# Kernel tuning notes

Hardware: AMD Instinct MI355X
Metric: run time of the kernel (lower is better)

## Reference

```python
import jax, jax.numpy as jnp
import numpy as np

B, T, U, D, V = 8, 200, 100, 512, 1024


def setup_inputs() -> dict:
    key = jax.random.key(0)
    k1, k2, k3, k4 = jax.random.split(key, 4)
    enc_out = jax.random.normal(k1, (B, T, D), dtype=jnp.float32)
    prefix = jax.random.randint(k2, (B, U), 0, V, dtype=jnp.int64)
    embedding = jax.random.normal(k3, (V, D), dtype=jnp.float32)
    joiner_w = jax.random.normal(k4, (V, D), dtype=jnp.float32) * (1.0 / np.sqrt(D))
    joiner_b = jnp.zeros((V,), dtype=jnp.float32)
    return {"enc_out": enc_out, "prefix": prefix, "embedding": embedding,
            "joiner_w": joiner_w, "joiner_b": joiner_b}


def reference(enc_out, prefix, embedding, joiner_w, joiner_b):
    # pred_emb: (B, U, D) via embedding lookup
    pred_emb = embedding[prefix]
    # broadcast add -> (B, T, U, D), then tanh
    joint = jnp.tanh(enc_out[:, :, None, :] + pred_emb[:, None, :, :])
    # linear projection to vocab: (B, T, U, V)
    logits = jnp.einsum('btud,vd->btuv', joint, joiner_w) + joiner_b
    return logits
```

## Files before the change

kernel.cpp:

```cpp
#include <hip/hip_runtime.h>

#define T_DIM 200
#define U_DIM 100
#define D_DIM 512
#define V_DIM 1024
#define TU_DIM (T_DIM * U_DIM)
#define M_TOTAL (8 * TU_DIM)
#define M_TILE 64

typedef __attribute__((ext_vector_type(8))) short bf16x8;
typedef __attribute__((ext_vector_type(4))) float f32x4;

__device__ __forceinline__ unsigned short f2bf(float f) {
    unsigned int u = __float_as_uint(f);
    u += 0x7FFFu + ((u >> 16) & 1u);
    return (unsigned short)(u >> 16);
}

__device__ __forceinline__ float fast_tanh(float x) {
    float e = __expf(2.0f * x);
    return 1.0f - 2.0f / (e + 1.0f);
}

__device__ __forceinline__ void row_ptrs(int g, const float* enc, const int* prefix,
                                         const float* emb, const float** encp, const float** embp) {
    const int b = g / TU_DIM;
    const int m = g - b * TU_DIM;
    const int t = m / U_DIM;
    const int u = m - t * U_DIM;
    *encp = enc + (size_t)(b * T_DIM + t) * D_DIM;
    *embp = emb + (size_t)prefix[b * U_DIM + u] * D_DIM;
}

__global__ void conv_w_kernel(const float* __restrict__ w, ushort4* __restrict__ wbf) {
    int i = blockIdx.x * blockDim.x + threadIdx.x;
    float4 v = reinterpret_cast<const float4*>(w)[i];
    ushort4 o;
    o.x = f2bf(v.x); o.y = f2bf(v.y); o.z = f2bf(v.z); o.w = f2bf(v.w);
    wbf[i] = o;
}

__global__ __launch_bounds__(512)
void mat_a_kernel(const float* __restrict__ enc, const int* __restrict__ prefix,
                  const float* __restrict__ emb, unsigned short* __restrict__ Abf) {
    const int tid = threadIdx.x;
    const int r = tid >> 3;
    const int q = tid & 7;
    const int rl = blockIdx.x * 64 + r;
    const float *encp, *embp;
    row_ptrs(rl, enc, prefix, emb, &encp, &embp);
    unsigned short* ap = Abf + (size_t)rl * D_DIM;
#pragma unroll
    for (int jj = 0; jj < 8; ++jj) {
        const int d = q * 8 + jj * 64;
        float4 e0 = *reinterpret_cast<const float4*>(encp + d);
        float4 e1 = *reinterpret_cast<const float4*>(encp + d + 4);
        float4 p0 = *reinterpret_cast<const float4*>(embp + d);
        float4 p1 = *reinterpret_cast<const float4*>(embp + d + 4);
        bf16x8 pk;
        pk[0] = (short)f2bf(fast_tanh(e0.x + p0.x));
        pk[1] = (short)f2bf(fast_tanh(e0.y + p0.y));
        pk[2] = (short)f2bf(fast_tanh(e0.z + p0.z));
        pk[3] = (short)f2bf(fast_tanh(e0.w + p0.w));
        pk[4] = (short)f2bf(fast_tanh(e1.x + p1.x));
        pk[5] = (short)f2bf(fast_tanh(e1.y + p1.y));
        pk[6] = (short)f2bf(fast_tanh(e1.z + p1.z));
        pk[7] = (short)f2bf(fast_tanh(e1.w + p1.w));
        *reinterpret_cast<bf16x8*>(&ap[d]) = pk;
    }
}

#define GLOAD_LDS16(gp, lp) \
    __builtin_amdgcn_global_load_lds( \
        (const __attribute__((address_space(1))) unsigned int*)(gp), \
        (__attribute__((address_space(3))) unsigned int*)(lp), 16, 0, 0)

__global__ __launch_bounds__(256, 2)
void gemm128_kernel(const unsigned short* __restrict__ Abf, const unsigned short* __restrict__ wbf,
                    const float* __restrict__ bias, float* __restrict__ out) {
    __shared__ unsigned short ldsA[2][128 * 64];
    __shared__ unsigned short ldsB[2][128 * 64];

    const int tid  = threadIdx.x;
    const int lane = tid & 63;
    const int wid  = tid >> 6;
    const int wm   = (wid >> 1) * 64;
    const int wn   = (wid & 1) * 64;
    const int lr   = lane & 15;
    const int lg   = lane >> 4;

    const int orig = blockIdx.x;
    const int wgid = (orig & 7) * 1250 + (orig >> 3);
    const int mt = wgid >> 3, nt = wgid & 7;
    const int row0 = mt * 128, col0 = nt * 128;

    const int rsub = tid >> 3;
    const int csw  = ((tid & 7) ^ (rsub & 7)) * 8;
    const unsigned short* aSt = Abf + (size_t)(row0 + rsub) * D_DIM + csw;
    const unsigned short* wSt = wbf + (size_t)(col0 + rsub) * D_DIM + csw;

    auto stage = [&](int buf, int kt) {
        const int k0 = kt * 64;
#pragma unroll
        for (int i = 0; i < 4; ++i)
            GLOAD_LDS16(aSt + (size_t)(i * 32) * D_DIM + k0,
                        &ldsA[buf][(i * 32 + wid * 8) * 64]);
#pragma unroll
        for (int i = 0; i < 4; ++i)
            GLOAD_LDS16(wSt + (size_t)(i * 32) * D_DIM + k0,
                        &ldsB[buf][(i * 32 + wid * 8) * 64]);
    };

    const unsigned short* ldsA0 = &ldsA[0][(wm + lr) * 64 + ((lg ^ (lr & 7)) * 8)];
    const unsigned short* ldsB0 = &ldsB[0][(wn + lr) * 64 + ((lg ^ (lr & 7)) * 8)];
    const int kk1off = ((((4 | lg) ^ (lr & 7)) - (lg ^ (lr & 7))) * 8);

    f32x4 acc[4][4];
#pragma unroll
    for (int mi = 0; mi < 4; ++mi)
#pragma unroll
        for (int ni = 0; ni < 4; ++ni)
            acc[mi][ni] = (f32x4){0.f, 0.f, 0.f, 0.f};

    auto compute = [&](int buf) {
        const unsigned short* pA = ldsA0 + buf * (128 * 64);
        const unsigned short* pB = ldsB0 + buf * (128 * 64);
#pragma unroll
        for (int kk = 0; kk < 2; ++kk) {
            const int ko = kk ? kk1off : 0;
            bf16x8 bfr[4];
#pragma unroll
            for (int ni = 0; ni < 4; ++ni)
                bfr[ni] = *reinterpret_cast<const bf16x8*>(pB + ni * (16 * 64) + ko);
            __builtin_amdgcn_s_setprio(1);
#pragma unroll
            for (int mi = 0; mi < 4; ++mi) {
                bf16x8 af = *reinterpret_cast<const bf16x8*>(pA + mi * (16 * 64) + ko);
#pragma unroll
                for (int ni = 0; ni < 4; ++ni)
                    acc[mi][ni] = __builtin_amdgcn_mfma_f32_16x16x32_bf16(af, bfr[ni], acc[mi][ni], 0, 0, 0);
            }
            __builtin_amdgcn_s_setprio(0);
        }
    };

    stage(0, 0);
    stage(1, 1);

#pragma unroll 1
    for (int it = 0; it < 4; ++it) {
        asm volatile("s_waitcnt vmcnt(8)" ::: "memory");
        __builtin_amdgcn_s_barrier();
        compute(0);
        asm volatile("s_waitcnt lgkmcnt(0)" ::: "memory");
        __builtin_amdgcn_s_barrier();
        if (it < 3) stage(0, 2 * it + 2);
        if (it < 3) asm volatile("s_waitcnt vmcnt(8)" ::: "memory");
        else        asm volatile("s_waitcnt vmcnt(0)" ::: "memory");
        __builtin_amdgcn_s_barrier();
        compute(1);
        if (it < 3) {
            asm volatile("s_waitcnt lgkmcnt(0)" ::: "memory");
            __builtin_amdgcn_s_barrier();
            stage(1, 2 * it + 3);
        }
    }

    float bv[4];
#pragma unroll
    for (int ni = 0; ni < 4; ++ni)
        bv[ni] = bias[col0 + wn + ni * 16 + lr];
#pragma unroll
    for (int mi = 0; mi < 4; ++mi) {
#pragma unroll
        for (int j = 0; j < 4; ++j) {
            const long long row = (long long)row0 + wm + mi * 16 + lg * 4 + j;
            float* op = out + row * V_DIM + col0 + wn;
#pragma unroll
            for (int ni = 0; ni < 4; ++ni)
                __builtin_nontemporal_store(acc[mi][ni][j] + bv[ni], &op[ni * 16 + lr]);
        }
    }
}

__global__ __launch_bounds__(512, 2)
void joiner_kernel(const float* __restrict__ enc, const int* __restrict__ prefix,
                   const float* __restrict__ emb, const unsigned short* __restrict__ wbf,
                   const float* __restrict__ bias, float* __restrict__ out) {
    __shared__ unsigned short A_s[M_TILE * 512];
    const int tid = threadIdx.x;
    const long long g0 = (long long)blockIdx.x * M_TILE;
    {
        const int r = tid >> 3, q = tid & 7;
        const float *encp, *embp;
        row_ptrs((int)g0 + r, enc, prefix, emb, &encp, &embp);
        const int r7 = r & 7;
#pragma unroll
        for (int jj = 0; jj < 8; ++jj) {
            const int d = q * 8 + jj * 64;
            float4 e0 = *reinterpret_cast<const float4*>(encp + d);
            float4 e1 = *reinterpret_cast<const float4*>(encp + d + 4);
            float4 p0 = *reinterpret_cast<const float4*>(embp + d);
            float4 p1 = *reinterpret_cast<const float4*>(embp + d + 4);
            bf16x8 pk;
            pk[0] = (short)f2bf(fast_tanh(e0.x + p0.x));
            pk[1] = (short)f2bf(fast_tanh(e0.y + p0.y));
            pk[2] = (short)f2bf(fast_tanh(e0.z + p0.z));
            pk[3] = (short)f2bf(fast_tanh(e0.w + p0.w));
            pk[4] = (short)f2bf(fast_tanh(e1.x + p1.x));
            pk[5] = (short)f2bf(fast_tanh(e1.y + p1.y));
            pk[6] = (short)f2bf(fast_tanh(e1.z + p1.z));
            pk[7] = (short)f2bf(fast_tanh(e1.w + p1.w));
            const int chunk = (q + 8 * jj) ^ r7;
            *reinterpret_cast<bf16x8*>(&A_s[r * 512 + chunk * 8]) = pk;
        }
    }
    __syncthreads();
    const int lane = tid & 63, wid = tid >> 6;
    const int wn = wid * 128, lr = lane & 15, lg = lane >> 4;
    const unsigned short* wb = wbf + (size_t)(wn + lr) * D_DIM + lg * 8;
    f32x4 acc[4][8];
#pragma unroll
    for (int mi = 0; mi < 4; ++mi)
#pragma unroll
        for (int ni = 0; ni < 8; ++ni) acc[mi][ni] = (f32x4){0.f, 0.f, 0.f, 0.f};
    bf16x8 bb[2][8];
#pragma unroll
    for (int ni = 0; ni < 8; ++ni)
        bb[0][ni] = *reinterpret_cast<const bf16x8*>(wb + ni * 16 * D_DIM);
#pragma unroll
    for (int s = 0; s < 16; ++s) {
        const int cur = s & 1, nxt = cur ^ 1;
        if (s < 15) {
#pragma unroll
            for (int ni = 0; ni < 8; ++ni)
                bb[nxt][ni] = *reinterpret_cast<const bf16x8*>(wb + ni * 16 * D_DIM + (s + 1) * 32);
        }
        bf16x8 af[4];
#pragma unroll
        for (int mi = 0; mi < 4; ++mi) {
            const int row = mi * 16 + lr;
            const int chunk = (s * 4 + lg) ^ (row & 7);
            af[mi] = *reinterpret_cast<const bf16x8*>(&A_s[row * 512 + chunk * 8]);
        }
#pragma unroll
        for (int mi = 0; mi < 4; ++mi)
#pragma unroll
            for (int ni = 0; ni < 8; ++ni)
                acc[mi][ni] = __builtin_amdgcn_mfma_f32_16x16x32_bf16(af[mi], bb[cur][ni], acc[mi][ni], 0, 0, 0);
    }
    float bv[8];
#pragma unroll
    for (int ni = 0; ni < 8; ++ni) bv[ni] = bias[wn + ni * 16 + lr];
#pragma unroll
    for (int mi = 0; mi < 4; ++mi) {
#pragma unroll
        for (int j = 0; j < 4; ++j) {
            const long long row = g0 + mi * 16 + lg * 4 + j;
            float* op = out + row * V_DIM + wn;
#pragma unroll
            for (int ni = 0; ni < 8; ++ni)
                op[ni * 16 + lr] = acc[mi][ni][j] + bv[ni];
        }
    }
}

extern "C" void kernel_launch(void* const* d_in, const int* in_sizes, int n_in,
                              void* d_out, int out_size, void* d_ws, size_t ws_size,
                              hipStream_t stream) {
    const float* enc    = (const float*)d_in[0];
    const int*   prefix = (const int*)d_in[1];
    const float* emb    = (const float*)d_in[2];
    const float* jw     = (const float*)d_in[3];
    const float* jb     = (const float*)d_in[4];
    float* out = (float*)d_out;

    unsigned short* wbf = (unsigned short*)d_ws;
    const size_t WB = (size_t)V_DIM * D_DIM * sizeof(unsigned short);
    const size_t AB = (size_t)M_TOTAL * D_DIM * sizeof(unsigned short);

    conv_w_kernel<<<512, 256, 0, stream>>>(jw, (ushort4*)wbf);

    if (ws_size >= WB + AB) {
        unsigned short* Abf = wbf + (size_t)V_DIM * D_DIM;
        mat_a_kernel<<<M_TOTAL / 64, 512, 0, stream>>>(enc, prefix, emb, Abf);
        gemm128_kernel<<<10000, 256, 0, stream>>>(Abf, wbf, jb, out);
    } else {
        joiner_kernel<<<M_TOTAL / M_TILE, 512, 0, stream>>>(enc, prefix, emb, wbf, jb, out);
    }
}
```

Baseline: 276.5 us.

## Prefetch whole LDS k-tile into registers before issuing next stage and MFMAs

The GEMM main loop now reads both k-halves of the A and B fragments for the current buffer into registers, then waits on LDS reads and immediately issues the global-to-LDS load for the next tile into the same buffer before running the MFMAs. This lets the next tile's global loads overlap the whole MFMA block and removes one barrier per tile. The cost is higher register pressure from holding 16 fragments. The tanh/bf16 pre-pass also switches its packed store to a nontemporal store.

```diff
diff --git a/kernel.cpp b/kernel.cpp
--- a/kernel.cpp
+++ b/kernel.cpp
@@ -66,7 +66,7 @@
         pk[5] = (short)f2bf(fast_tanh(e1.y + p1.y));
         pk[6] = (short)f2bf(fast_tanh(e1.z + p1.z));
         pk[7] = (short)f2bf(fast_tanh(e1.w + p1.w));
-        *reinterpret_cast<bf16x8*>(&ap[d]) = pk;
+        __builtin_nontemporal_store(pk, reinterpret_cast<bf16x8*>(&ap[d]));
     }
 }
 
@@ -122,47 +122,45 @@
         for (int ni = 0; ni < 4; ++ni)
             acc[mi][ni] = (f32x4){0.f, 0.f, 0.f, 0.f};
 
-    auto compute = [&](int buf) {
+    stage(0, 0);
+    stage(1, 1);
+    asm volatile("s_waitcnt vmcnt(8)" ::: "memory");
+    __builtin_amdgcn_s_barrier();
+
+#pragma unroll 1
+    for (int it = 0; it < 8; ++it) {
+        const int buf = it & 1;
         const unsigned short* pA = ldsA0 + buf * (128 * 64);
         const unsigned short* pB = ldsB0 + buf * (128 * 64);
+        bf16x8 fa[2][4], fb[2][4];
 #pragma unroll
         for (int kk = 0; kk < 2; ++kk) {
             const int ko = kk ? kk1off : 0;
-            bf16x8 bfr[4];
+#pragma unroll
+            for (int mi = 0; mi < 4; ++mi)
+                fa[kk][mi] = *reinterpret_cast<const bf16x8*>(pA + mi * (16 * 64) + ko);
 #pragma unroll
             for (int ni = 0; ni < 4; ++ni)
-                bfr[ni] = *reinterpret_cast<const bf16x8*>(pB + ni * (16 * 64) + ko);
-            __builtin_amdgcn_s_setprio(1);
-#pragma unroll
-            for (int mi = 0; mi < 4; ++mi) {
-                bf16x8 af = *reinterpret_cast<const bf16x8*>(pA + mi * (16 * 64) + ko);
-#pragma unroll
-                for (int ni = 0; ni < 4; ++ni)
-                    acc[mi][ni] = __builtin_amdgcn_mfma_f32_16x16x32_bf16(af, bfr[ni], acc[mi][ni], 0, 0, 0);
-            }
-            __builtin_amdgcn_s_setprio(0);
-        }
-    };
-
-    stage(0, 0);
-    stage(1, 1);
-
-#pragma unroll 1
-    for (int it = 0; it < 4; ++it) {
-        asm volatile("s_waitcnt vmcnt(8)" ::: "memory");
-        __builtin_amdgcn_s_barrier();
-        compute(0);
+                fb[kk][ni] = *reinterpret_cast<const bf16x8*>(pB + ni * (16 * 64) + ko);
+        }
         asm volatile("s_waitcnt lgkmcnt(0)" ::: "memory");
         __builtin_amdgcn_s_barrier();
-        if (it < 3) stage(0, 2 * it + 2);
-        if (it < 3) asm volatile("s_waitcnt vmcnt(8)" ::: "memory");
-        else        asm volatile("s_waitcnt vmcnt(0)" ::: "memory");
-        __builtin_amdgcn_s_barrier();
-        compute(1);
-        if (it < 3) {
-            asm volatile("s_waitcnt lgkmcnt(0)" ::: "memory");
+        if (it < 6) stage(buf, it + 2);
+        __builtin_amdgcn_s_setprio(1);
+#pragma unroll
+        for (int kk = 0; kk < 2; ++kk)
+#pragma unroll
+            for (int mi = 0; mi < 4; ++mi)
+#pragma unroll
+                for (int ni = 0; ni < 4; ++ni)
+                    acc[mi][ni] = __builtin_amdgcn_mfma_f32_16x16x32_bf16(fa[kk][mi], fb[kk][ni], acc[mi][ni], 0, 0, 0);
+        __builtin_amdgcn_s_setprio(0);
+        if (it < 6) {
+            asm volatile("s_waitcnt vmcnt(8)" ::: "memory");
             __builtin_amdgcn_s_barrier();
-            stage(1, 2 * it + 3);
+        } else if (it == 6) {
+            asm volatile("s_waitcnt vmcnt(0)" ::: "memory");
+            __builtin_amdgcn_s_barrier();
         }
     }
 
```

New measurement: 383.7 us. 1.39x slower.

## Fuse weight conversion, activation prep and GEMM into one cooperative persistent kernel

Applied to the files above, without the earlier changes.

Replaces the three launches (weight bf16 conversion, tanh activation matrix build, tiled GEMM) with a single cooperative kernel of 512 persistent blocks. The blocks do the conversion and the A-matrix build, synchronise with a grid-wide barrier, then loop over the GEMM tiles. The output stores become nontemporal. This removes launch gaps and tail effects between stages, in exchange for a grid sync and fewer resident blocks, which may lower latency hiding in the GEMM phase. The old launch path remains as a fallback if the cooperative launch fails.

```diff
diff --git a/kernel.cpp b/kernel.cpp
--- a/kernel.cpp
+++ b/kernel.cpp
@@ -1,4 +1,7 @@
 #include <hip/hip_runtime.h>
+#include <hip/hip_cooperative_groups.h>
+
+namespace cg = cooperative_groups;
 
 #define T_DIM 200
 #define U_DIM 100
@@ -7,6 +10,8 @@
 #define TU_DIM (T_DIM * U_DIM)
 #define M_TOTAL (8 * TU_DIM)
 #define M_TILE 64
+#define NTILES 10000
+#define PBLK 512
 
 typedef __attribute__((ext_vector_type(8))) short bf16x8;
 typedef __attribute__((ext_vector_type(4))) float f32x4;
@@ -30,6 +35,162 @@
     const int u = m - t * U_DIM;
     *encp = enc + (size_t)(b * T_DIM + t) * D_DIM;
     *embp = emb + (size_t)prefix[b * U_DIM + u] * D_DIM;
+}
+
+__device__ __forceinline__ void mat_a_row8(const float* encp, const float* embp,
+                                           unsigned short* ap, int d) {
+    float4 e0 = *reinterpret_cast<const float4*>(encp + d);
+    float4 e1 = *reinterpret_cast<const float4*>(encp + d + 4);
+    float4 p0 = *reinterpret_cast<const float4*>(embp + d);
+    float4 p1 = *reinterpret_cast<const float4*>(embp + d + 4);
+    bf16x8 pk;
+    pk[0] = (short)f2bf(fast_tanh(e0.x + p0.x));
+    pk[1] = (short)f2bf(fast_tanh(e0.y + p0.y));
+    pk[2] = (short)f2bf(fast_tanh(e0.z + p0.z));
+    pk[3] = (short)f2bf(fast_tanh(e0.w + p0.w));
+    pk[4] = (short)f2bf(fast_tanh(e1.x + p1.x));
+    pk[5] = (short)f2bf(fast_tanh(e1.y + p1.y));
+    pk[6] = (short)f2bf(fast_tanh(e1.z + p1.z));
+    pk[7] = (short)f2bf(fast_tanh(e1.w + p1.w));
+    *reinterpret_cast<bf16x8*>(&ap[d]) = pk;
+}
+
+#define GLOAD_LDS16(gp, lp) \
+    __builtin_amdgcn_global_load_lds( \
+        (const __attribute__((address_space(1))) unsigned int*)(gp), \
+        (__attribute__((address_space(3))) unsigned int*)(lp), 16, 0, 0)
+
+__global__ __launch_bounds__(256, 2)
+void fused_kernel(const float* __restrict__ enc, const int* __restrict__ prefix,
+                  const float* __restrict__ emb, const float* __restrict__ w,
+                  const float* __restrict__ bias, float* __restrict__ out,
+                  unsigned short* __restrict__ wbf, unsigned short* __restrict__ Abf) {
+    __shared__ unsigned short ldsA[2][128 * 64];
+    __shared__ unsigned short ldsB[2][128 * 64];
+
+    const int tid  = threadIdx.x;
+    const int lane = tid & 63;
+    const int wid  = tid >> 6;
+    const int wm   = (wid >> 1) * 64;
+    const int wn   = (wid & 1) * 64;
+    const int lr   = lane & 15;
+    const int lg   = lane >> 4;
+
+    {
+        const int i = blockIdx.x * 256 + tid;
+        float4 v = reinterpret_cast<const float4*>(w)[i];
+        ushort4 o;
+        o.x = f2bf(v.x); o.y = f2bf(v.y); o.z = f2bf(v.z); o.w = f2bf(v.w);
+        reinterpret_cast<ushort4*>(wbf)[i] = o;
+        const int rsub8 = tid >> 3;
+        const int q = tid & 7;
+        for (int g = blockIdx.x; g < 5000; g += PBLK) {
+            const int rl = g * 32 + rsub8;
+            const float *encp, *embp;
+            row_ptrs(rl, enc, prefix, emb, &encp, &embp);
+            unsigned short* ap = Abf + (size_t)rl * D_DIM;
+#pragma unroll
+            for (int jj = 0; jj < 8; ++jj)
+                mat_a_row8(encp, embp, ap, q * 8 + jj * 64);
+        }
+    }
+    __threadfence();
+    cg::this_grid().sync();
+
+    const int rsub = tid >> 3;
+    const int csw  = ((tid & 7) ^ (rsub & 7)) * 8;
+    const unsigned short* ldsA0 = &ldsA[0][(wm + lr) * 64 + ((lg ^ (lr & 7)) * 8)];
+    const unsigned short* ldsB0 = &ldsB[0][(wn + lr) * 64 + ((lg ^ (lr & 7)) * 8)];
+    const int kk1off = ((((4 | lg) ^ (lr & 7)) - (lg ^ (lr & 7))) * 8);
+
+#pragma unroll 1
+    for (int tile = blockIdx.x; tile < NTILES; tile += PBLK) {
+        const int wgid = (tile & 7) * 1250 + (tile >> 3);
+        const int mt = wgid >> 3, nt = wgid & 7;
+        const int row0 = mt * 128, col0 = nt * 128;
+
+        const unsigned short* aSt = Abf + (size_t)(row0 + rsub) * D_DIM + csw;
+        const unsigned short* wSt = wbf + (size_t)(col0 + rsub) * D_DIM + csw;
+
+        auto stage = [&](int buf, int kt) {
+            const int k0 = kt * 64;
+#pragma unroll
+            for (int i = 0; i < 4; ++i)
+                GLOAD_LDS16(aSt + (size_t)(i * 32) * D_DIM + k0,
+                            &ldsA[buf][(i * 32 + wid * 8) * 64]);
+#pragma unroll
+            for (int i = 0; i < 4; ++i)
+                GLOAD_LDS16(wSt + (size_t)(i * 32) * D_DIM + k0,
+                            &ldsB[buf][(i * 32 + wid * 8) * 64]);
+        };
+
+        f32x4 acc[4][4];
+#pragma unroll
+        for (int mi = 0; mi < 4; ++mi)
+#pragma unroll
+            for (int ni = 0; ni < 4; ++ni)
+                acc[mi][ni] = (f32x4){0.f, 0.f, 0.f, 0.f};
+
+        auto compute = [&](int buf) {
+            const unsigned short* pA = ldsA0 + buf * (128 * 64);
+            const unsigned short* pB = ldsB0 + buf * (128 * 64);
+#pragma unroll
+            for (int kk = 0; kk < 2; ++kk) {
+                const int ko = kk ? kk1off : 0;
+                bf16x8 bfr[4];
+#pragma unroll
+                for (int ni = 0; ni < 4; ++ni)
+                    bfr[ni] = *reinterpret_cast<const bf16x8*>(pB + ni * (16 * 64) + ko);
+                __builtin_amdgcn_s_setprio(1);
+#pragma unroll
+                for (int mi = 0; mi < 4; ++mi) {
+                    bf16x8 af = *reinterpret_cast<const bf16x8*>(pA + mi * (16 * 64) + ko);
+#pragma unroll
+                    for (int ni = 0; ni < 4; ++ni)
+                        acc[mi][ni] = __builtin_amdgcn_mfma_f32_16x16x32_bf16(af, bfr[ni], acc[mi][ni], 0, 0, 0);
+                }
+                __builtin_amdgcn_s_setprio(0);
+            }
+        };
+
+        stage(0, 0);
+        stage(1, 1);
+#pragma unroll 1
+        for (int it = 0; it < 4; ++it) {
+            asm volatile("s_waitcnt vmcnt(8)" ::: "memory");
+            __builtin_amdgcn_s_barrier();
+            compute(0);
+            asm volatile("s_waitcnt lgkmcnt(0)" ::: "memory");
+            __builtin_amdgcn_s_barrier();
+            if (it < 3) stage(0, 2 * it + 2);
+            if (it < 3) asm volatile("s_waitcnt vmcnt(8)" ::: "memory");
+            else        asm volatile("s_waitcnt vmcnt(0)" ::: "memory");
+            __builtin_amdgcn_s_barrier();
+            compute(1);
+            if (it < 3) {
+                asm volatile("s_waitcnt lgkmcnt(0)" ::: "memory");
+                __builtin_amdgcn_s_barrier();
+                stage(1, 2 * it + 3);
+            }
+        }
+
+        float bv[4];
+#pragma unroll
+        for (int ni = 0; ni < 4; ++ni)
+            bv[ni] = bias[col0 + wn + ni * 16 + lr];
+#pragma unroll
+        for (int mi = 0; mi < 4; ++mi) {
+#pragma unroll
+            for (int j = 0; j < 4; ++j) {
+                const long long row = (long long)row0 + wm + mi * 16 + lg * 4 + j;
+                float* op = out + row * V_DIM + col0 + wn;
+#pragma unroll
+                for (int ni = 0; ni < 4; ++ni)
+                    __builtin_nontemporal_store(acc[mi][ni][j] + bv[ni], &op[ni * 16 + lr]);
+            }
+        }
+        __builtin_amdgcn_s_barrier();
+    }
 }
 
 __global__ void conv_w_kernel(const float* __restrict__ w, ushort4* __restrict__ wbf) {
@@ -51,29 +212,9 @@
     row_ptrs(rl, enc, prefix, emb, &encp, &embp);
     unsigned short* ap = Abf + (size_t)rl * D_DIM;
 #pragma unroll
-    for (int jj = 0; jj < 8; ++jj) {
-        const int d = q * 8 + jj * 64;
-        float4 e0 = *reinterpret_cast<const float4*>(encp + d);
-        float4 e1 = *reinterpret_cast<const float4*>(encp + d + 4);
-        float4 p0 = *reinterpret_cast<const float4*>(embp + d);
-        float4 p1 = *reinterpret_cast<const float4*>(embp + d + 4);
-        bf16x8 pk;
-        pk[0] = (short)f2bf(fast_tanh(e0.x + p0.x));
-        pk[1] = (short)f2bf(fast_tanh(e0.y + p0.y));
-        pk[2] = (short)f2bf(fast_tanh(e0.z + p0.z));
-        pk[3] = (short)f2bf(fast_tanh(e0.w + p0.w));
-        pk[4] = (short)f2bf(fast_tanh(e1.x + p1.x));
-        pk[5] = (short)f2bf(fast_tanh(e1.y + p1.y));
-        pk[6] = (short)f2bf(fast_tanh(e1.z + p1.z));
-        pk[7] = (short)f2bf(fast_tanh(e1.w + p1.w));
-        *reinterpret_cast<bf16x8*>(&ap[d]) = pk;
-    }
-}
-
-#define GLOAD_LDS16(gp, lp) \
-    __builtin_amdgcn_global_load_lds( \
-        (const __attribute__((address_space(1))) unsigned int*)(gp), \
-        (__attribute__((address_space(3))) unsigned int*)(lp), 16, 0, 0)
+    for (int jj = 0; jj < 8; ++jj)
+        mat_a_row8(encp, embp, ap, q * 8 + jj * 64);
+}
 
 __global__ __launch_bounds__(256, 2)
 void gemm128_kernel(const unsigned short* __restrict__ Abf, const unsigned short* __restrict__ wbf,
@@ -278,14 +419,20 @@
     unsigned short* wbf = (unsigned short*)d_ws;
     const size_t WB = (size_t)V_DIM * D_DIM * sizeof(unsigned short);
     const size_t AB = (size_t)M_TOTAL * D_DIM * sizeof(unsigned short);
-
-    conv_w_kernel<<<512, 256, 0, stream>>>(jw, (ushort4*)wbf);
+    unsigned short* Abf = wbf + (size_t)V_DIM * D_DIM;
 
     if (ws_size >= WB + AB) {
-        unsigned short* Abf = wbf + (size_t)V_DIM * D_DIM;
-        mat_a_kernel<<<M_TOTAL / 64, 512, 0, stream>>>(enc, prefix, emb, Abf);
-        gemm128_kernel<<<10000, 256, 0, stream>>>(Abf, wbf, jb, out);
+        void* args[] = {(void*)&enc, (void*)&prefix, (void*)&emb, (void*)&jw,
+                        (void*)&jb,  (void*)&out,    (void*)&wbf, (void*)&Abf};
+        hipError_t err = hipLaunchCooperativeKernel((const void*)fused_kernel,
+                                                    dim3(PBLK), dim3(256), args, 0, stream);
+        if (err != hipSuccess) {
+            conv_w_kernel<<<512, 256, 0, stream>>>(jw, (ushort4*)wbf);
+            mat_a_kernel<<<M_TOTAL / 64, 512, 0, stream>>>(enc, prefix, emb, Abf);
+            gemm128_kernel<<<NTILES, 256, 0, stream>>>(Abf, wbf, jb, out);
+        }
     } else {
+        conv_w_kernel<<<512, 256, 0, stream>>>(jw, (ushort4*)wbf);
         joiner_kernel<<<M_TOTAL / M_TILE, 512, 0, stream>>>(enc, prefix, emb, wbf, jb, out);
     }
 }
```

Result: slower. 398.4 us (+44.1%).
